# Kernel tuning notes

Measured on AMD Instinct MI355X. Metric: run time of the kernel, lower is better.

The kernel has to match this reference:

```python
import jax, jax.numpy as jnp
import numpy as np
from jax import lax

B = 1024          # batch size (queries / docs)
H = 1536          # GRU hidden = embedding dim (hard-coded in module)
MAX_NEGS = 32     # max negatives per query
TEMP = 0.05       # opt.temperature


def setup_inputs() -> dict:
    key = jax.random.key(0)
    ks = jax.random.split(key, 8)
    rng = np.random.default_rng(0)
    lens = rng.integers(0, MAX_NEGS + 1, size=B)  # variable-length negs, some zero
    total = int(lens.sum())
    s = 0.02
    return {
        "q_emb": jax.random.normal(ks[0], (B, H), jnp.float32),
        "k_emb": jax.random.normal(ks[1], (B, H), jnp.float32),
        "inpn_emb": jax.random.normal(ks[2], (total, H), jnp.float32),
        "len_input_negs": jnp.asarray(lens, jnp.int32),
        "W_ih": jax.random.normal(ks[3], (3 * H, H), jnp.float32) * s,
        "W_hh": jax.random.normal(ks[4], (3 * H, H), jnp.float32) * s,
        "b_ih": jax.random.normal(ks[5], (3 * H,), jnp.float32) * s,
        "b_hh": jax.random.normal(ks[6], (3 * H,), jnp.float32) * s,
    }


def _ragged_gru_final(inpn_emb, lens, h0, W_ih, W_hh, b_ih, b_hh):
    """Batched equivalent of the per-sample torch GRU loop.

    For sample i: run a 1-layer GRU over inpn_emb[start_i:start_i+len_i]
    with initial hidden h0[i]; return final hidden (h0[i] if len_i == 0).
    """
    total = inpn_emb.shape[0]
    offsets = jnp.concatenate([jnp.zeros((1,), jnp.int32),
                               jnp.cumsum(lens)[:-1].astype(jnp.int32)])
    t = jnp.arange(MAX_NEGS, dtype=jnp.int32)
    idx = jnp.clip(offsets[:, None] + t[None, :], 0, total - 1)   # [B, Lmax]
    mask = t[None, :] < lens[:, None]                              # [B, Lmax]
    x_pad = inpn_emb[idx]                                          # [B, Lmax, H]

    def step(h, xm):
        x, m = xm                                  # x: [B,H], m: [B]
        gi = x @ W_ih.T + b_ih                     # [B, 3H]
        gh = h @ W_hh.T + b_hh                     # [B, 3H]
        i_r, i_z, i_n = jnp.split(gi, 3, axis=-1)
        h_r, h_z, h_n = jnp.split(gh, 3, axis=-1)
        r = jax.nn.sigmoid(i_r + h_r)
        z = jax.nn.sigmoid(i_z + h_z)
        n = jnp.tanh(i_n + r * h_n)
        h_new = (1.0 - z) * n + z * h
        h = jnp.where(m[:, None], h_new, h)        # freeze past end of seq
        return h, None

    h_final, _ = lax.scan(step, h0,
                          (x_pad.transpose(1, 0, 2), mask.T))
    return h_final


def reference(q_emb, k_emb, inpn_emb, len_input_negs, W_ih, W_hh, b_ih, b_hh):
    qemb = _ragged_gru_final(inpn_emb, len_input_negs, q_emb,
                             W_ih, W_hh, b_ih, b_hh)          # [B, H]
    scores = jnp.einsum("id,jd->ij", qemb / TEMP, k_emb)       # [B, B]
    labels = jnp.arange(B)
    logp = jax.nn.log_softmax(scores, axis=-1)
    loss = -jnp.mean(jnp.take_along_axis(logp, labels[:, None], axis=1))
    return loss
```

## Files before the change

### kernel.cpp

```cpp
#include <hip/hip_runtime.h>
#include <hip/hip_bf16.h>

#define B_SZ 1024
#define H_DIM 1536
#define H3 (3*H_DIM)
#define LMAX 32
#define TEMP_INV 20.0f

typedef __attribute__((ext_vector_type(4))) float f32x4;
typedef __attribute__((ext_vector_type(8))) short short8;
typedef unsigned short u16;
typedef unsigned int u32;

__device__ __forceinline__ u16 f2bf(float f){
  union { float f; u32 u; } v; v.f = f;
  u32 r = (v.u + 0x7FFFu + ((v.u >> 16) & 1u)) >> 16;
  return (u16)r;
}
__device__ __forceinline__ u32 pack2(float lo, float hi){
  return (u32)f2bf(lo) | ((u32)f2bf(hi) << 16);
}
__device__ __forceinline__ float bf2f(u16 b){
  union { u32 u; float f; } v; v.u = ((u32)b) << 16; return v.f;
}
__device__ __forceinline__ float sigm(float x){ return 1.f / (1.f + __expf(-x)); }

__device__ __forceinline__ void gload_lds16(const void* g, void* l){
  __builtin_amdgcn_global_load_lds(
      (const __attribute__((address_space(1))) void*)g,
      (__attribute__((address_space(3))) void*)l, 16, 0, 0);
}

__global__ void sort_kernel(const int* __restrict__ lens, int* __restrict__ rank,
                            int* __restrict__ cnt_arr, int* __restrict__ tstart,
                            int* __restrict__ rowmap)
{
  __shared__ int wavecnt[33][17];
  __shared__ int bintot[33];
  __shared__ int scnt[LMAX];
  __shared__ int sts[LMAX];
  __shared__ int soff[B_SZ];
  int i = threadIdx.x;
  int li = lens[i];
  int w = i >> 6, lane = i & 63;

  if (i < 33 * 17) ((int*)wavecnt)[i] = 0;
  __syncthreads();

  int mypre = 0;
  #pragma unroll 1
  for (int b = 0; b <= 32; ++b) {
    unsigned long long m = __ballot(li == b);
    if (lane == 0) wavecnt[b][w] = __popcll(m);
    if (b == li) mypre = __popcll(m & ((1ull << lane) - 1ull));
  }
  __syncthreads();

  if (i < 33) {
    int c = 0;
    #pragma unroll 1
    for (int w2 = 0; w2 < 16; ++w2) c += wavecnt[i][w2];
    bintot[i] = c;
  }
  __syncthreads();

  int wpre = 0;
  #pragma unroll 1
  for (int w2 = 0; w2 < w; ++w2) wpre += wavecnt[li][w2];
  int base = 0;
  #pragma unroll 1
  for (int b = li + 1; b <= 32; ++b) base += bintot[b];
  int r = base + wpre + mypre;
  rank[i] = r;

  if (i < LMAX) {
    int c = 0;
    #pragma unroll 1
    for (int b = i + 1; b <= 32; ++b) c += bintot[b];
    scnt[i] = c; cnt_arr[i] = c;
  }
  __syncthreads();
  if (i == 0) {
    int acc = 0;
    for (int t = 0; t < LMAX; ++t) { sts[t] = acc; tstart[t] = acc; acc += scnt[t]; }
  }

  soff[i] = li;
  __syncthreads();
  for (int off = 1; off < B_SZ; off <<= 1) {
    int v = (i >= off) ? soff[i - off] : 0;
    __syncthreads();
    soff[i] += v;
    __syncthreads();
  }
  int myoff = soff[i] - li;
  for (int t = 0; t < li; ++t)
    rowmap[myoff + t] = sts[t] + r;
}

__global__ void prep_kernel(const float* __restrict__ wih, const float* __restrict__ whh,
                            const float* __restrict__ kemb, const float* __restrict__ qemb,
                            const int* __restrict__ rank,
                            u16* __restrict__ wih_bf, u16* __restrict__ whh_bf,
                            u16* __restrict__ k_bf, u16* __restrict__ h0)
{
  size_t o = ((size_t)blockIdx.x * 256 + threadIdx.x) * 8;
  if (o < (size_t)H3 * H_DIM) {
    float4 a0 = *(const float4*)(wih + o), a1 = *(const float4*)(wih + o + 4);
    *(uint4*)(wih_bf + o) = make_uint4(pack2(a0.x,a0.y), pack2(a0.z,a0.w),
                                       pack2(a1.x,a1.y), pack2(a1.z,a1.w));
    float4 b0 = *(const float4*)(whh + o), b1 = *(const float4*)(whh + o + 4);
    *(uint4*)(whh_bf + o) = make_uint4(pack2(b0.x,b0.y), pack2(b0.z,b0.w),
                                       pack2(b1.x,b1.y), pack2(b1.z,b1.w));
  }
  if (o < (size_t)B_SZ * H_DIM) {
    float4 k0 = *(const float4*)(kemb + o), k1 = *(const float4*)(kemb + o + 4);
    *(uint4*)(k_bf + o) = make_uint4(pack2(k0.x,k0.y), pack2(k0.z,k0.w),
                                     pack2(k1.x,k1.y), pack2(k1.z,k1.w));
    int i = (int)(o / H_DIM), col = (int)(o % H_DIM);
    float4 q0 = *(const float4*)(qemb + o), q1 = *(const float4*)(qemb + o + 4);
    *(uint4*)(h0 + (size_t)rank[i] * H_DIM + col) =
        make_uint4(pack2(q0.x,q0.y), pack2(q0.z,q0.w),
                   pack2(q1.x,q1.y), pack2(q1.z,q1.w));
  }
}

__global__ void convx_kernel(const float* __restrict__ x, const int* __restrict__ rowmap,
                             u16* __restrict__ xt, int total){
  size_t o = ((size_t)blockIdx.x * 256 + threadIdx.x) * 8;
  int row = (int)(o / H_DIM), col = (int)(o % H_DIM);
  if (row < total) {
    float4 a0 = *(const float4*)(x + o), a1 = *(const float4*)(x + o + 4);
    *(uint4*)(xt + (size_t)rowmap[row] * H_DIM + col) =
        make_uint4(pack2(a0.x,a0.y), pack2(a0.z,a0.w),
                   pack2(a1.x,a1.y), pack2(a1.z,a1.w));
  } else {
    *(uint4*)(xt + o) = make_uint4(0,0,0,0);
  }
}

__global__ __launch_bounds__(512, 2) void gi_gemm_kernel(
    const u16* __restrict__ x_bf, const u16* __restrict__ wih_bf,
    const float* __restrict__ b_ih, u16* __restrict__ gi, int mt)
{
  int nblk = mt * 18;
  int id = blockIdx.x;
  int q8 = nblk >> 3, r8 = nblk & 7;
  int xcd = id & 7, off = id >> 3;
  int swz = (xcd < r8) ? (xcd * (q8 + 1) + off) : (r8 * (q8 + 1) + (xcd - r8) * q8 + off);
  int bx = swz / 18, by = swz % 18;

  __shared__ u16 lds[2 * 32768];
  char* ldsb = (char*)lds;

  int tid = threadIdx.x, wid = tid >> 6, lane = tid & 63;
  int wm = wid >> 2, wn = wid & 3;
  int lrow = lane & 15, lkh = lane >> 4;

  f32x4 acc[8][4] = {};

  auto SH = [&](int dbuf, int which, int tile){
    char* base = ldsb + dbuf * 65536 + which * 16384;
    int k0 = tile * 64;
    #pragma unroll
    for (int it = 0; it < 2; ++it) {
      int cb = wid * 128 + it * 64;
      int c  = cb + lane;
      int row = c >> 3, slot = c & 7;
      const u16* src;
      if (which < 2) src = x_bf   + (size_t)(bx * 256 + which * 128 + row) * H_DIM;
      else           src = wih_bf + (size_t)(by * 256 + (which - 2) * 128 + row) * H_DIM;
      src += k0 + ((slot ^ (row & 7)) << 3);
      gload_lds16(src, base + (size_t)cb * 16);
    }
  };

  SH(0,2,0); SH(0,3,0); SH(0,0,0); SH(0,1,0); SH(1,2,1); SH(1,3,1);
  asm volatile("s_waitcnt vmcnt(4)" ::: "memory");
  __builtin_amdgcn_sched_barrier(0);
  __builtin_amdgcn_s_barrier();
  __builtin_amdgcn_sched_barrier(0);

  short8 bfr[4][2], afr[2][2];

  for (int k = 0; k < 24; ++k) {
    int d = k & 1;
    char* Ab = ldsb + d * 65536 + wm * 16384;
    char* Bb = ldsb + d * 65536 + 32768 + (wn >> 1) * 16384;
    int bloc = (wn & 1) * 64;

    #pragma unroll
    for (int cf = 0; cf < 4; ++cf)
      #pragma unroll
      for (int ks = 0; ks < 2; ++ks) {
        int r = bloc + cf * 16 + lrow;
        bfr[cf][ks] = *(const short8*)(Bb + r * 128 + (((ks*4+lkh) ^ (r & 7)) << 4));
      }
    #pragma unroll
    for (int rq = 0; rq < 2; ++rq)
      #pragma unroll
      for (int ks = 0; ks < 2; ++ks) {
        int r = rq * 16 + lrow;
        afr[rq][ks] = *(const short8*)(Ab + r * 128 + (((ks*4+lkh) ^ (r & 7)) << 4));
      }
    if (k + 1 < 24) SH(d ^ 1, 0, k + 1);
    __builtin_amdgcn_s_setprio(1);
    #pragma unroll
    for (int rq = 0; rq < 2; ++rq)
      #pragma unroll
      for (int cf = 0; cf < 4; ++cf)
        #pragma unroll
        for (int ks = 0; ks < 2; ++ks)
          acc[rq][cf] = __builtin_amdgcn_mfma_f32_16x16x32_bf16(
              afr[rq][ks], bfr[cf][ks], acc[rq][cf], 0, 0, 0);
    __builtin_amdgcn_s_setprio(0);
    __builtin_amdgcn_s_barrier();
    __builtin_amdgcn_sched_barrier(0);

    #pragma unroll
    for (int q = 1; q < 4; ++q) {
      #pragma unroll
      for (int rq = 0; rq < 2; ++rq)
        #pragma unroll
        for (int ks = 0; ks < 2; ++ks) {
          int r = (q * 2 + rq) * 16 + lrow;
          afr[rq][ks] = *(const short8*)(Ab + r * 128 + (((ks*4+lkh) ^ (r & 7)) << 4));
        }
      if (q == 1) {
        if (k + 1 < 24) SH(d ^ 1, 1, k + 1);
        if (k + 2 < 24) SH(d,     2, k + 2);
      } else if (q == 2) {
        if (k + 2 < 24) SH(d,     3, k + 2);
      }
      __builtin_amdgcn_s_setprio(1);
      #pragma unroll
      for (int rq = 0; rq < 2; ++rq)
        #pragma unroll
        for (int cf = 0; cf < 4; ++cf)
          #pragma unroll
          for (int ks = 0; ks < 2; ++ks)
            acc[q*2+rq][cf] = __builtin_amdgcn_mfma_f32_16x16x32_bf16(
                afr[rq][ks], bfr[cf][ks], acc[q*2+rq][cf], 0, 0, 0);
      __builtin_amdgcn_s_setprio(0);
      if (q == 3) {
        if (k < 22) asm volatile("s_waitcnt vmcnt(4)" ::: "memory");
        else        asm volatile("s_waitcnt vmcnt(0)" ::: "memory");
        __builtin_amdgcn_sched_barrier(0);
      }
      __builtin_amdgcn_s_barrier();
      __builtin_amdgcn_sched_barrier(0);
    }
  }

  #pragma unroll
  for (int cf = 0; cf < 4; ++cf) {
    int j = by * 256 + wn * 64 + cf * 16 + lrow;
    float bias = b_ih[j];
    #pragma unroll
    for (int rf = 0; rf < 8; ++rf)
      #pragma unroll
      for (int r4 = 0; r4 < 4; ++r4) {
        int rowg = bx * 256 + wm * 128 + rf * 16 + lkh * 4 + r4;
        gi[(size_t)rowg * 4608 + j] = f2bf(acc[rf][cf][r4] + bias);
      }
  }
}

__global__ __launch_bounds__(256, 4) void gh_step_kernel(
    const u16* __restrict__ h_cur, u16* __restrict__ h_nxt,
    const u16* __restrict__ whh_bf, const u16* __restrict__ gi,
    const float* __restrict__ b_hh,
    const int* __restrict__ cnt_arr, const int* __restrict__ tstart, int t)
{
  int cnt = cnt_arr[t];
  int bid = blockIdx.x;
  int x8 = bid & 7, jj = bid >> 3;
  int ct = x8 * 6 + jj % 6;
  int bx = jj / 6;
  if (bx * 64 >= cnt) return;
  int ts = tstart[t];

  __shared__ u16 lds[2 * 10240];
  char* ldsb = (char*)lds;

  int tid = threadIdx.x, wid = tid >> 6, lane = tid & 63;
  int wm = wid >> 1, wn = wid & 1;
  int lrow = lane & 15, lkh = lane >> 4;
  f32x4 acc[3][2] = {};
  float hold[2][4];

  auto STAGE = [&](int buf, int kt){
    int k0 = kt * 64;
    char* base = ldsb + buf * 20480;
    #pragma unroll
    for (int it = 0; it < 5; ++it) {
      int cb = it * 256 + wid * 64;
      int c  = cb + lane;
      const u16* src;
      if (c < 512) {
        int row = c >> 3, slot = c & 7;
        int ridx = bx * 64 + row; if (ridx >= cnt) ridx = cnt - 1;
        src = h_cur + (size_t)ridx * H_DIM + k0 + ((slot ^ (row & 7)) << 3);
      } else {
        int w = c - 512;
        int slab = w >> 8, row = (w >> 3) & 31, slot = w & 7;
        src = whh_bf + (size_t)(slab * H_DIM + ct * 32 + row) * H_DIM
              + k0 + ((slot ^ (row & 7)) << 3);
      }
      gload_lds16(src, base + (size_t)cb * 16);
    }
  };

  auto COMPUTE = [&](int buf){
    char* base = ldsb + buf * 20480;
    #pragma unroll
    for (int qq = 0; qq < 2; ++qq) {
      short8 ah[2], bw[3];
      int slot = qq * 4 + lkh;
      #pragma unroll
      for (int m = 0; m < 2; ++m) {
        int row = wm * 32 + m * 16 + lrow;
        ah[m] = *(const short8*)(base + row * 128 + ((slot ^ (row & 7)) << 4));
      }
      {
        int row = wn * 16 + lrow;
        int byte = row * 128 + ((slot ^ (row & 7)) << 4);
        #pragma unroll
        for (int s = 0; s < 3; ++s)
          bw[s] = *(const short8*)(base + 8192 + s * 4096 + byte);
      }
      #pragma unroll
      for (int s = 0; s < 3; ++s)
        #pragma unroll
        for (int m = 0; m < 2; ++m)
          acc[s][m] = __builtin_amdgcn_mfma_f32_16x16x32_bf16(
              ah[m], bw[s], acc[s][m], 0, 0, 0);
    }
  };

  STAGE(0, 0);

  int lc = wn * 16 + lrow;
  int j = ct * 32 + lc;
  u16 pgir[2][4], pgiz[2][4], pgin[2][4];
  asm volatile("" ::: "memory");
  float bhr = b_hh[j], bhz = b_hh[H_DIM + j], bhn = b_hh[2*H_DIM + j];
  #pragma unroll
  for (int m = 0; m < 2; ++m)
    #pragma unroll
    for (int r4 = 0; r4 < 4; ++r4) {
      int lm = wm * 32 + m * 16 + lkh * 4 + r4;
      int ridx = bx * 64 + lm; if (ridx >= cnt) ridx = cnt - 1;
      size_t gr = (size_t)(ts + ridx) * 4608;
      pgir[m][r4] = __builtin_nontemporal_load(&gi[gr + j]);
      pgiz[m][r4] = __builtin_nontemporal_load(&gi[gr + H_DIM + j]);
      pgin[m][r4] = __builtin_nontemporal_load(&gi[gr + 2*H_DIM + j]);
    }
  asm volatile("" ::: "memory");

  for (int kt = 0; kt < 24; ++kt) {
    if (kt + 1 < 24) {
      STAGE((kt + 1) & 1, kt + 1);
      asm volatile("s_waitcnt vmcnt(5)" ::: "memory");
    } else {
      asm volatile("s_waitcnt vmcnt(0)" ::: "memory");
    }
    __builtin_amdgcn_sched_barrier(0);
    __builtin_amdgcn_s_barrier();
    __builtin_amdgcn_sched_barrier(0);
    COMPUTE(kt & 1);
    if (kt == (ct >> 1)) {
      char* base = ldsb + (kt & 1) * 20480;
      int col = ((ct & 1) << 5) + wn * 16 + lrow;
      int slot = col >> 3, within = col & 7;
      #pragma unroll
      for (int m = 0; m < 2; ++m)
        #pragma unroll
        for (int r4 = 0; r4 < 4; ++r4) {
          int row = wm * 32 + m * 16 + lkh * 4 + r4;
          hold[m][r4] = bf2f(*(const u16*)(base + row * 128 +
                             ((slot ^ (row & 7)) << 4) + within * 2));
        }
    }
    __builtin_amdgcn_s_barrier();
    __builtin_amdgcn_sched_barrier(0);
  }

  #pragma unroll
  for (int m = 0; m < 2; ++m)
    #pragma unroll
    for (int r4 = 0; r4 < 4; ++r4) {
      int lm = wm * 32 + m * 16 + lkh * 4 + r4;
      int ridx = bx * 64 + lm;
      if (ridx < cnt) {
        float rr = sigm(bf2f(pgir[m][r4]) + acc[0][m][r4] + bhr);
        float zz = sigm(bf2f(pgiz[m][r4]) + acc[1][m][r4] + bhz);
        float nn = tanhf(bf2f(pgin[m][r4]) + rr * (acc[2][m][r4] + bhn));
        h_nxt[(size_t)ridx * H_DIM + j] = f2bf((1.f - zz) * nn + zz * hold[m][r4]);
      }
    }
}

__global__ __launch_bounds__(256, 2) void scores_kernel(
    const u16* __restrict__ h0, const u16* __restrict__ h1,
    const int* __restrict__ lens, const int* __restrict__ rank,
    const u16* __restrict__ k_bf, float* __restrict__ scores)
{
  int bx = blockIdx.x, by = blockIdx.y;
  __shared__ u16 lds[2 * 2 * 64 * 64];
  char* ldsb = (char*)lds;
  int tid = threadIdx.x, wid = tid >> 6, lane = tid & 63;
  int wm = wid >> 1, wn = wid & 1;
  int lrow = lane & 15, lkh = lane >> 4;
  f32x4 acc[2][2] = {};

  auto STAGE = [&](int buf, int kt){
    int k0 = kt * 64;
    char* base = ldsb + buf * 16384;
    #pragma unroll
    for (int it = 0; it < 4; ++it) {
      int cb = it * 256 + wid * 64;
      int c  = cb + lane;
      int isB = c >> 9;
      int cc  = c & 511;
      int row = cc >> 3, slot = cc & 7;
      const u16* src;
      if (!isB) {
        int g = bx * 64 + row;
        src = ((lens[g] & 1) ? h1 : h0) + (size_t)rank[g] * H_DIM;
      } else {
        src = k_bf + (size_t)(by * 64 + row) * H_DIM;
      }
      src += k0 + ((slot ^ (row & 7)) << 3);
      gload_lds16(src, base + (size_t)cb * 16);
    }
  };

  auto COMPUTE = [&](int buf){
    char* base = ldsb + buf * 16384;
    #pragma unroll
    for (int qq = 0; qq < 2; ++qq) {
      short8 a[2], b[2];
      int slot = qq * 4 + lkh;
      #pragma unroll
      for (int m = 0; m < 2; ++m) {
        int row = wm * 32 + m * 16 + lrow;
        a[m] = *(const short8*)(base + row * 128 + ((slot ^ (row & 7)) << 4));
      }
      #pragma unroll
      for (int n = 0; n < 2; ++n) {
        int row = wn * 32 + n * 16 + lrow;
        b[n] = *(const short8*)(base + 8192 + row * 128 + ((slot ^ (row & 7)) << 4));
      }
      #pragma unroll
      for (int m = 0; m < 2; ++m)
        #pragma unroll
        for (int n = 0; n < 2; ++n)
          acc[m][n] = __builtin_amdgcn_mfma_f32_16x16x32_bf16(a[m], b[n], acc[m][n], 0,0,0);
    }
  };

  STAGE(0, 0);
  for (int kt = 0; kt < 24; ++kt) {
    if (kt + 1 < 24) {
      STAGE((kt + 1) & 1, kt + 1);
      asm volatile("s_waitcnt vmcnt(4)" ::: "memory");
    } else {
      asm volatile("s_waitcnt vmcnt(0)" ::: "memory");
    }
    __builtin_amdgcn_sched_barrier(0);
    __builtin_amdgcn_s_barrier();
    __builtin_amdgcn_sched_barrier(0);
    COMPUTE(kt & 1);
    __builtin_amdgcn_s_barrier();
    __builtin_amdgcn_sched_barrier(0);
  }
  #pragma unroll
  for (int m = 0; m < 2; ++m)
    #pragma unroll
    for (int n = 0; n < 2; ++n) {
      int col = by * 64 + wn * 32 + n * 16 + lrow;
      #pragma unroll
      for (int r4 = 0; r4 < 4; ++r4) {
        int rowg = bx * 64 + wm * 32 + m * 16 + lkh * 4 + r4;
        scores[(size_t)rowg * B_SZ + col] = acc[m][n][r4] * TEMP_INV;
      }
    }
}

__global__ void softmax_kernel(const float* __restrict__ scores, float* __restrict__ out){
  int i = blockIdx.x;
  int tid = threadIdx.x;
  const float* row = scores + (size_t)i * B_SZ;
  __shared__ float red[4];
  float m = -INFINITY;
  for (int j = tid; j < B_SZ; j += 256) m = fmaxf(m, row[j]);
  for (int off = 32; off; off >>= 1) m = fmaxf(m, __shfl_xor(m, off));
  if ((tid & 63) == 0) red[tid >> 6] = m;
  __syncthreads();
  m = fmaxf(fmaxf(red[0], red[1]), fmaxf(red[2], red[3]));
  __syncthreads();
  float s = 0.f;
  for (int j = tid; j < B_SZ; j += 256) s += __expf(row[j] - m);
  for (int off = 32; off; off >>= 1) s += __shfl_xor(s, off);
  if ((tid & 63) == 0) red[tid >> 6] = s;
  __syncthreads();
  if (tid == 0) {
    float S = red[0] + red[1] + red[2] + red[3];
    atomicAdd(out, (m + __logf(S) - row[i]) * (1.0f / B_SZ));
  }
}

extern "C" void kernel_launch(void* const* d_in, const int* in_sizes, int n_in,
                              void* d_out, int out_size, void* d_ws, size_t ws_size,
                              hipStream_t stream) {
  const float* q_emb = (const float*)d_in[0];
  const float* k_emb = (const float*)d_in[1];
  const float* inpn  = (const float*)d_in[2];
  const int*   lens  = (const int*)d_in[3];
  const float* wih   = (const float*)d_in[4];
  const float* whh   = (const float*)d_in[5];
  const float* bih   = (const float*)d_in[6];
  const float* bhh   = (const float*)d_in[7];
  float* out = (float*)d_out;

  int total  = in_sizes[2] / H_DIM;
  int mtiles = (total + 255) / 256;
  int Mpad   = mtiles * 256;

  char* p = (char*)d_ws;
  auto alloc = [&](size_t bytes){ char* r = p; p += (bytes + 255) & ~(size_t)255; return r; };
  int* rank      = (int*)alloc(B_SZ * 4);
  int* cnt_arr   = (int*)alloc(LMAX * 4);
  int* tstart    = (int*)alloc(LMAX * 4);
  int* rowmap    = (int*)alloc((size_t)Mpad * 4);
  u16* hbuf0     = (u16*)alloc((size_t)B_SZ * H_DIM * 2);
  u16* hbuf1     = (u16*)alloc((size_t)B_SZ * H_DIM * 2);
  u16* wih_bf    = (u16*)alloc((size_t)H3 * H_DIM * 2);
  u16* whh_bf    = (u16*)alloc((size_t)H3 * H_DIM * 2);
  u16* k_bf      = (u16*)alloc((size_t)B_SZ * H_DIM * 2);
  u16* xt        = (u16*)alloc((size_t)Mpad * H_DIM * 2);
  u16* gi        = (u16*)alloc((size_t)Mpad * H3 * 2);
  float* scores  = (float*)alloc((size_t)B_SZ * B_SZ * 4);
  if ((size_t)(p - (char*)d_ws) > ws_size) return;

  hipMemsetAsync(out, 0, 4, stream);

  sort_kernel<<<1, B_SZ, 0, stream>>>(lens, rank, cnt_arr, tstart, rowmap);
  prep_kernel<<<(H3 * H_DIM / 8) / 256, 256, 0, stream>>>(
      wih, whh, k_emb, q_emb, rank, wih_bf, whh_bf, k_bf, hbuf0);
  convx_kernel<<<((size_t)Mpad * H_DIM / 8) / 256, 256, 0, stream>>>(
      inpn, rowmap, xt, total);

  gi_gemm_kernel<<<mtiles * 18, 512, 0, stream>>>(xt, wih_bf, bih, gi, mtiles);

  for (int t = 0; t < LMAX; ++t) {
    u16* hc = (t & 1) ? hbuf1 : hbuf0;
    u16* hn = (t & 1) ? hbuf0 : hbuf1;
    int cmax = total / (t + 1); if (cmax > B_SZ) cmax = B_SZ;
    if (cmax <= 0) break;
    int tiles = (cmax + 63) / 64;
    gh_step_kernel<<<48 * tiles, 256, 0, stream>>>(
        hc, hn, whh_bf, gi, bhh, cnt_arr, tstart, t);
  }

  scores_kernel<<<dim3(B_SZ / 64, B_SZ / 64), 256, 0, stream>>>(
      hbuf0, hbuf1, lens, rank, k_bf, scores);
  softmax_kernel<<<B_SZ, 256, 0, stream>>>(scores, out);
}
```

Before: 928.1 us.

## Run recurrent GRU hidden-state GEMM in FP8 with scaled weights and hidden state

Converts W_hh to FP8 (scaled by 64) and keeps a parallel FP8 copy of the hidden state (scaled by 4), then switches the per-step recurrent GEMM to fp8 MFMA with half the LDS staging traffic. The previous hidden value for the gate update is now read directly from the bf16 buffer instead of extracted from LDS. This targets the 32 sequential step kernels' memory and compute cost, at the cost of reduced precision in the recurrent term and an extra FP8 store per step.

```diff
diff --git a/kernel.cpp b/kernel.cpp
--- a/kernel.cpp
+++ b/kernel.cpp
@@ -11,6 +11,7 @@
 typedef __attribute__((ext_vector_type(8))) short short8;
 typedef unsigned short u16;
 typedef unsigned int u32;
+typedef unsigned char u8;
 
 __device__ __forceinline__ u16 f2bf(float f){
   union { float f; u32 u; } v; v.f = f;
@@ -29,6 +30,11 @@
   __builtin_amdgcn_global_load_lds(
       (const __attribute__((address_space(1))) void*)g,
       (__attribute__((address_space(3))) void*)l, 16, 0, 0);
+}
+__device__ __forceinline__ u32 pk_fp8x4(float a, float b, float c, float d){
+  u32 r = __builtin_amdgcn_cvt_pk_fp8_f32(a, b, 0, false);
+  r = __builtin_amdgcn_cvt_pk_fp8_f32(c, d, r, true);
+  return r;
 }
 
 __global__ void sort_kernel(const int* __restrict__ lens, int* __restrict__ rank,
@@ -101,8 +107,9 @@
 __global__ void prep_kernel(const float* __restrict__ wih, const float* __restrict__ whh,
                             const float* __restrict__ kemb, const float* __restrict__ qemb,
                             const int* __restrict__ rank,
-                            u16* __restrict__ wih_bf, u16* __restrict__ whh_bf,
-                            u16* __restrict__ k_bf, u16* __restrict__ h0)
+                            u16* __restrict__ wih_bf, u8* __restrict__ whh8,
+                            u16* __restrict__ k_bf, u16* __restrict__ h0,
+                            u8* __restrict__ h80)
 {
   size_t o = ((size_t)blockIdx.x * 256 + threadIdx.x) * 8;
   if (o < (size_t)H3 * H_DIM) {
@@ -110,8 +117,9 @@
     *(uint4*)(wih_bf + o) = make_uint4(pack2(a0.x,a0.y), pack2(a0.z,a0.w),
                                        pack2(a1.x,a1.y), pack2(a1.z,a1.w));
     float4 b0 = *(const float4*)(whh + o), b1 = *(const float4*)(whh + o + 4);
-    *(uint4*)(whh_bf + o) = make_uint4(pack2(b0.x,b0.y), pack2(b0.z,b0.w),
-                                       pack2(b1.x,b1.y), pack2(b1.z,b1.w));
+    *(uint2*)(whh8 + o) = make_uint2(
+        pk_fp8x4(b0.x*64.f, b0.y*64.f, b0.z*64.f, b0.w*64.f),
+        pk_fp8x4(b1.x*64.f, b1.y*64.f, b1.z*64.f, b1.w*64.f));
   }
   if (o < (size_t)B_SZ * H_DIM) {
     float4 k0 = *(const float4*)(kemb + o), k1 = *(const float4*)(kemb + o + 4);
@@ -119,9 +127,12 @@
                                      pack2(k1.x,k1.y), pack2(k1.z,k1.w));
     int i = (int)(o / H_DIM), col = (int)(o % H_DIM);
     float4 q0 = *(const float4*)(qemb + o), q1 = *(const float4*)(qemb + o + 4);
-    *(uint4*)(h0 + (size_t)rank[i] * H_DIM + col) =
-        make_uint4(pack2(q0.x,q0.y), pack2(q0.z,q0.w),
-                   pack2(q1.x,q1.y), pack2(q1.z,q1.w));
+    size_t ro = (size_t)rank[i] * H_DIM + col;
+    *(uint4*)(h0 + ro) = make_uint4(pack2(q0.x,q0.y), pack2(q0.z,q0.w),
+                                    pack2(q1.x,q1.y), pack2(q1.z,q1.w));
+    *(uint2*)(h80 + ro) = make_uint2(
+        pk_fp8x4(q0.x*4.f, q0.y*4.f, q0.z*4.f, q0.w*4.f),
+        pk_fp8x4(q1.x*4.f, q1.y*4.f, q1.z*4.f, q1.w*4.f));
   }
 }
 
@@ -268,7 +279,8 @@
 
 __global__ __launch_bounds__(256, 4) void gh_step_kernel(
     const u16* __restrict__ h_cur, u16* __restrict__ h_nxt,
-    const u16* __restrict__ whh_bf, const u16* __restrict__ gi,
+    const u8* __restrict__ h8_cur, u8* __restrict__ h8_nxt,
+    const u8* __restrict__ whh8, const u16* __restrict__ gi,
     const float* __restrict__ b_hh,
     const int* __restrict__ cnt_arr, const int* __restrict__ tstart, int t)
 {
@@ -280,60 +292,62 @@
   if (bx * 64 >= cnt) return;
   int ts = tstart[t];
 
-  __shared__ u16 lds[2 * 10240];
-  char* ldsb = (char*)lds;
+  __shared__ char lds[2 * 10240];
+  char* ldsb = lds;
 
   int tid = threadIdx.x, wid = tid >> 6, lane = tid & 63;
   int wm = wid >> 1, wn = wid & 1;
   int lrow = lane & 15, lkh = lane >> 4;
   f32x4 acc[3][2] = {};
-  float hold[2][4];
 
   auto STAGE = [&](int buf, int kt){
     int k0 = kt * 64;
-    char* base = ldsb + buf * 20480;
-    #pragma unroll
-    for (int it = 0; it < 5; ++it) {
-      int cb = it * 256 + wid * 64;
+    char* base = ldsb + buf * 10240;
+    #pragma unroll
+    for (int it = 0; it < 3; ++it) {
+      int cb = wid * 160 + it * 64;
       int c  = cb + lane;
-      const u16* src;
-      if (c < 512) {
-        int row = c >> 3, slot = c & 7;
-        int ridx = bx * 64 + row; if (ridx >= cnt) ridx = cnt - 1;
-        src = h_cur + (size_t)ridx * H_DIM + k0 + ((slot ^ (row & 7)) << 3);
-      } else {
-        int w = c - 512;
-        int slab = w >> 8, row = (w >> 3) & 31, slot = w & 7;
-        src = whh_bf + (size_t)(slab * H_DIM + ct * 32 + row) * H_DIM
-              + k0 + ((slot ^ (row & 7)) << 3);
-      }
-      gload_lds16(src, base + (size_t)cb * 16);
+      if (it < 2 || lane < 32) {
+        const u8* src;
+        if (c < 256) {
+          int row = c >> 2, s16 = c & 3;
+          int ridx = bx * 64 + row; if (ridx >= cnt) ridx = cnt - 1;
+          src = h8_cur + (size_t)ridx * H_DIM + k0 + ((s16 ^ (row & 3)) << 4);
+        } else {
+          int w = c - 256;
+          int slab = w >> 7, row = (w >> 2) & 31, s16 = w & 3;
+          src = whh8 + (size_t)(slab * H_DIM + ct * 32 + row) * H_DIM
+                + k0 + ((s16 ^ (row & 3)) << 4);
+        }
+        gload_lds16(src, base + (size_t)cb * 16);
+      }
     }
   };
 
   auto COMPUTE = [&](int buf){
-    char* base = ldsb + buf * 20480;
+    char* base = ldsb + buf * 10240;
     #pragma unroll
     for (int qq = 0; qq < 2; ++qq) {
-      short8 ah[2], bw[3];
-      int slot = qq * 4 + lkh;
+      int slot8 = qq * 4 + lkh;
+      int s16 = slot8 >> 1, sub = (slot8 & 1) << 3;
+      long ah[2], bw[3];
       #pragma unroll
       for (int m = 0; m < 2; ++m) {
         int row = wm * 32 + m * 16 + lrow;
-        ah[m] = *(const short8*)(base + row * 128 + ((slot ^ (row & 7)) << 4));
+        ah[m] = *(const long*)(base + row * 64 + ((s16 ^ (row & 3)) << 4) + sub);
       }
       {
         int row = wn * 16 + lrow;
-        int byte = row * 128 + ((slot ^ (row & 7)) << 4);
+        int off = row * 64 + ((s16 ^ (row & 3)) << 4) + sub;
         #pragma unroll
         for (int s = 0; s < 3; ++s)
-          bw[s] = *(const short8*)(base + 8192 + s * 4096 + byte);
+          bw[s] = *(const long*)(base + 4096 + s * 2048 + off);
       }
       #pragma unroll
       for (int s = 0; s < 3; ++s)
         #pragma unroll
         for (int m = 0; m < 2; ++m)
-          acc[s][m] = __builtin_amdgcn_mfma_f32_16x16x32_bf16(
+          acc[s][m] = __builtin_amdgcn_mfma_f32_16x16x32_fp8_fp8(
               ah[m], bw[s], acc[s][m], 0, 0, 0);
     }
   };
@@ -342,7 +356,7 @@
 
   int lc = wn * 16 + lrow;
   int j = ct * 32 + lc;
-  u16 pgir[2][4], pgiz[2][4], pgin[2][4];
+  u16 pgir[2][4], pgiz[2][4], pgin[2][4], pgh[2][4];
   asm volatile("" ::: "memory");
   float bhr = b_hh[j], bhz = b_hh[H_DIM + j], bhn = b_hh[2*H_DIM + j];
   #pragma unroll
@@ -355,13 +369,14 @@
       pgir[m][r4] = __builtin_nontemporal_load(&gi[gr + j]);
       pgiz[m][r4] = __builtin_nontemporal_load(&gi[gr + H_DIM + j]);
       pgin[m][r4] = __builtin_nontemporal_load(&gi[gr + 2*H_DIM + j]);
+      pgh[m][r4]  = h_cur[(size_t)ridx * H_DIM + j];
     }
   asm volatile("" ::: "memory");
 
   for (int kt = 0; kt < 24; ++kt) {
     if (kt + 1 < 24) {
       STAGE((kt + 1) & 1, kt + 1);
-      asm volatile("s_waitcnt vmcnt(5)" ::: "memory");
+      asm volatile("s_waitcnt vmcnt(3)" ::: "memory");
     } else {
       asm volatile("s_waitcnt vmcnt(0)" ::: "memory");
     }
@@ -369,23 +384,11 @@
     __builtin_amdgcn_s_barrier();
     __builtin_amdgcn_sched_barrier(0);
     COMPUTE(kt & 1);
-    if (kt == (ct >> 1)) {
-      char* base = ldsb + (kt & 1) * 20480;
-      int col = ((ct & 1) << 5) + wn * 16 + lrow;
-      int slot = col >> 3, within = col & 7;
-      #pragma unroll
-      for (int m = 0; m < 2; ++m)
-        #pragma unroll
-        for (int r4 = 0; r4 < 4; ++r4) {
-          int row = wm * 32 + m * 16 + lkh * 4 + r4;
-          hold[m][r4] = bf2f(*(const u16*)(base + row * 128 +
-                             ((slot ^ (row & 7)) << 4) + within * 2));
-        }
-    }
     __builtin_amdgcn_s_barrier();
     __builtin_amdgcn_sched_barrier(0);
   }
 
+  const float S = 1.f / 256.f;
   #pragma unroll
   for (int m = 0; m < 2; ++m)
     #pragma unroll
@@ -393,10 +396,14 @@
       int lm = wm * 32 + m * 16 + lkh * 4 + r4;
       int ridx = bx * 64 + lm;
       if (ridx < cnt) {
-        float rr = sigm(bf2f(pgir[m][r4]) + acc[0][m][r4] + bhr);
-        float zz = sigm(bf2f(pgiz[m][r4]) + acc[1][m][r4] + bhz);
-        float nn = tanhf(bf2f(pgin[m][r4]) + rr * (acc[2][m][r4] + bhn));
-        h_nxt[(size_t)ridx * H_DIM + j] = f2bf((1.f - zz) * nn + zz * hold[m][r4]);
+        float rr = sigm(bf2f(pgir[m][r4]) + acc[0][m][r4] * S + bhr);
+        float zz = sigm(bf2f(pgiz[m][r4]) + acc[1][m][r4] * S + bhz);
+        float nn = tanhf(bf2f(pgin[m][r4]) + rr * (acc[2][m][r4] * S + bhn));
+        float hnew = (1.f - zz) * nn + zz * bf2f(pgh[m][r4]);
+        size_t idx = (size_t)ridx * H_DIM + j;
+        h_nxt[idx] = f2bf(hnew);
+        u32 p = __builtin_amdgcn_cvt_pk_fp8_f32(hnew * 4.f, 0.f, 0, false);
+        h8_nxt[idx] = (u8)(p & 0xff);
       }
     }
 }
@@ -536,8 +543,10 @@
   int* rowmap    = (int*)alloc((size_t)Mpad * 4);
   u16* hbuf0     = (u16*)alloc((size_t)B_SZ * H_DIM * 2);
   u16* hbuf1     = (u16*)alloc((size_t)B_SZ * H_DIM * 2);
+  u8*  h8buf0    = (u8*)alloc((size_t)B_SZ * H_DIM);
+  u8*  h8buf1    = (u8*)alloc((size_t)B_SZ * H_DIM);
   u16* wih_bf    = (u16*)alloc((size_t)H3 * H_DIM * 2);
-  u16* whh_bf    = (u16*)alloc((size_t)H3 * H_DIM * 2);
+  u8*  whh8      = (u8*)alloc((size_t)H3 * H_DIM);
   u16* k_bf      = (u16*)alloc((size_t)B_SZ * H_DIM * 2);
   u16* xt        = (u16*)alloc((size_t)Mpad * H_DIM * 2);
   u16* gi        = (u16*)alloc((size_t)Mpad * H3 * 2);
@@ -548,7 +557,7 @@
 
   sort_kernel<<<1, B_SZ, 0, stream>>>(lens, rank, cnt_arr, tstart, rowmap);
   prep_kernel<<<(H3 * H_DIM / 8) / 256, 256, 0, stream>>>(
-      wih, whh, k_emb, q_emb, rank, wih_bf, whh_bf, k_bf, hbuf0);
+      wih, whh, k_emb, q_emb, rank, wih_bf, whh8, k_bf, hbuf0, h8buf0);
   convx_kernel<<<((size_t)Mpad * H_DIM / 8) / 256, 256, 0, stream>>>(
       inpn, rowmap, xt, total);
 
@@ -557,11 +566,13 @@
   for (int t = 0; t < LMAX; ++t) {
     u16* hc = (t & 1) ? hbuf1 : hbuf0;
     u16* hn = (t & 1) ? hbuf0 : hbuf1;
+    u8*  hc8 = (t & 1) ? h8buf1 : h8buf0;
+    u8*  hn8 = (t & 1) ? h8buf0 : h8buf1;
     int cmax = total / (t + 1); if (cmax > B_SZ) cmax = B_SZ;
     if (cmax <= 0) break;
     int tiles = (cmax + 63) / 64;
     gh_step_kernel<<<48 * tiles, 256, 0, stream>>>(
-        hc, hn, whh_bf, gi, bhh, cnt_arr, tstart, t);
+        hc, hn, hc8, hn8, whh8, gi, bhh, cnt_arr, tstart, t);
   }
 
   scores_kernel<<<dim3(B_SZ / 64, B_SZ / 64), 256, 0, stream>>>(
```

Result: slower. 1.005 ms (+8.3%).
